# Performance work log

Hardware: AMD Instinct MI355X
Metric: run time of the kernel (lower is better)

The kernel has to match this reference:

```python
import jax, jax.numpy as jnp
import numpy as np

B, S, D, H = 2, 2048, 1024, 16
HW = D // H  # head width = 64
MASK_FILL = -100000000.0


def setup_inputs() -> dict:
    key0 = jax.random.key(0)
    ks = jax.random.split(key0, 12)
    inp = {
        "query": jax.random.normal(ks[0], (B, S, D), jnp.float32),
        "key": jax.random.normal(ks[1], (B, S, D), jnp.float32),
        "value": jax.random.normal(ks[2], (B, S, D), jnp.float32),
        # bool mask, True masks; broadcasts over batch and heads
        "mask": jax.random.randint(ks[3], (S, S), 0, 2).astype(jnp.bool_),
        # per-head projection kernels: (heads, head_width, d_in)
        "Wq": jax.random.normal(ks[4], (H, HW, D), jnp.float32) * 0.02,
        "bq": jnp.zeros((H, HW), jnp.float32),
        "Wk": jax.random.normal(ks[5], (H, HW, D), jnp.float32) * 0.02,
        "bk": jnp.zeros((H, HW), jnp.float32),
        "Wv": jax.random.normal(ks[6], (H, HW, D), jnp.float32) * 0.02,
        "bv": jnp.zeros((H, HW), jnp.float32),
        # collapse projector: contracts (heads, head_width) -> d_output
        "Wo": jax.random.normal(ks[7], (D, H, HW), jnp.float32) * 0.02,
        "bo": jnp.zeros((D,), jnp.float32),
    }
    return inp


def reference(query, key, value, mask, Wq, bq, Wk, bk, Wv, bv, Wo, bo):
    # head projections -> (b, h, s, w)
    q = jnp.einsum("bsd,hwd->bhsw", query, Wq) + bq[:, None, :]
    k = jnp.einsum("btd,hwd->bhtw", key, Wk) + bk[:, None, :]
    v = jnp.einsum("btd,hwd->bhtw", value, Wv) + bv[:, None, :]
    # unscaled logits, masked_fill, softmax (matches original exactly)
    logits = jnp.einsum("bhsw,bhtw->bhst", q, k)
    logits = jnp.where(mask, MASK_FILL, logits)
    score = jax.nn.softmax(logits, axis=-1)
    # NOTE: original divides AV output by sqrt(head_width) AFTER softmax
    attn = jnp.einsum("bhst,bhtw->bhsw", score, v) / jnp.sqrt(jnp.float32(HW))
    # collapse heads -> (b, s, d_output)
    out = jnp.einsum("bhsw,ohw->bso", attn, Wo) + bo
    return out
```

## Files before the change

kernel.cpp:

```cpp
#include <hip/hip_runtime.h>
#include <hip/hip_bf16.h>
#include <math.h>

#define S_LEN   2048
#define D_MODEL 1024
#define N_HEADS 16
#define HEAD_W  64
#define BATCH   2
#define MROWS   (BATCH * S_LEN)
#define MASK_FILL -100000000.0f
#define LOG2E 1.4426950408889634f

typedef __attribute__((ext_vector_type(8))) short bf16x8;
typedef __attribute__((ext_vector_type(4))) float f32x4;
typedef unsigned short u16;
typedef unsigned int   u32;
typedef unsigned long long u64;

__device__ __forceinline__ u16 f2bf(float f) {
    u32 u = __float_as_uint(f);
    return (u16)((u + 0x7fffu + ((u >> 16) & 1u)) >> 16);
}

__device__ __forceinline__ u32 pack_bf16x2(float lo, float hi) {
    __hip_bfloat162 t = __float22bfloat162_rn(make_float2(lo, hi));
    u32 r;
    __builtin_memcpy(&r, &t, 4);
    return r;
}

__device__ __forceinline__ void gld_lds16(const void* gp, void* lp) {
    __builtin_amdgcn_global_load_lds(
        (const __attribute__((address_space(1))) u32*)gp,
        (__attribute__((address_space(3))) u32*)lp, 16, 0, 0);
}

struct CvtJobs {
    const float* src[7];
    u16* dst[7];
    int n[7];
};
__global__ __launch_bounds__(256) void prep_kernel(
    CvtJobs j, const unsigned char* __restrict__ mask, u64* __restrict__ bits) {
    const int t = blockIdx.y;
    if (t < 7) {
        const float* s = j.src[t];
        u16* d = j.dst[t];
        const int n = j.n[t];
        int i = (blockIdx.x * 256 + threadIdx.x) * 4;
        if (i < n) {
            float4 v = *(const float4*)(s + i);
            ushort4 o;
            o.x = f2bf(v.x); o.y = f2bf(v.y); o.z = f2bf(v.z); o.w = f2bf(v.w);
            *(ushort4*)(d + i) = o;
        }
        return;
    }
    if (blockIdx.x >= 2048) return;
    __shared__ int isByte;
    if (threadIdx.x == 0) isByte = 0;
    __syncthreads();
    const int e0 = blockIdx.x * 2048;
    const uint2 v = ((const uint2*)(mask + e0))[threadIdx.x];
    if (((v.x | v.y) & 0xFFFFFF00u) != 0u) isByte = 1;
    __syncthreads();
    const int ib = isByte;
    const int* mi = (const int*)mask;
#pragma unroll
    for (int jj = 0; jj < 8; ++jj) {
        const int e = e0 + jj * 256 + threadIdx.x;
        const bool m = ib ? (mask[e] != 0) : (mi[e] != 0);
        const u64 bl = __ballot(m);
        if ((e & 63) == 0) bits[e >> 6] = bl;
    }
}

__device__ __forceinline__ void gemm_core_bf16(const u16* __restrict__ A,
                                               const u16* __restrict__ Bt,
                                               int m0, int n0, f32x4 acc[4][4]) {
    __shared__ u16 As[2][4096];
    __shared__ u16 Bs[2][4096];
    const int tid = threadIdx.x;
    const int wv = tid >> 6, ln = tid & 63;
    const int lane16 = ln & 15, quad = ln >> 4;
    const int wr = (wv >> 1) * 64, wc = (wv & 1) * 64;
    const u16* A0 = A + (size_t)(m0 + ln) * D_MODEL + wv * 8;
    const u16* A1 = A + (size_t)(m0 + 64 + ln) * D_MODEL + wv * 8;
    const u16* B0 = Bt + (size_t)(n0 + ln) * D_MODEL + wv * 8;
    const u16* B1 = Bt + (size_t)(n0 + 64 + ln) * D_MODEL + wv * 8;

    gld_lds16(A0, &As[0][wv * 1024]);
    gld_lds16(A1, &As[0][wv * 1024 + 512]);
    gld_lds16(B0, &Bs[0][wv * 1024]);
    gld_lds16(B1, &Bs[0][wv * 1024 + 512]);

    for (int kt = 0; kt < D_MODEL / 32; ++kt) {
        const int buf = kt & 1;
        __syncthreads();
        if (kt < D_MODEL / 32 - 1) {
            const int ko = (kt + 1) * 32;
            gld_lds16(A0 + ko, &As[buf ^ 1][wv * 1024]);
            gld_lds16(A1 + ko, &As[buf ^ 1][wv * 1024 + 512]);
            gld_lds16(B0 + ko, &Bs[buf ^ 1][wv * 1024]);
            gld_lds16(B1 + ko, &Bs[buf ^ 1][wv * 1024 + 512]);
        }
        bf16x8 af[4], bfv[4];
#pragma unroll
        for (int mt = 0; mt < 4; ++mt)
            af[mt] = *(const bf16x8*)&As[buf][quad * 1024 + (wr + mt * 16 + lane16) * 8];
#pragma unroll
        for (int nt = 0; nt < 4; ++nt)
            bfv[nt] = *(const bf16x8*)&Bs[buf][quad * 1024 + (wc + nt * 16 + lane16) * 8];
#pragma unroll
        for (int mt = 0; mt < 4; ++mt)
#pragma unroll
            for (int nt = 0; nt < 4; ++nt)
                acc[mt][nt] = __builtin_amdgcn_mfma_f32_16x16x32_bf16(
                    af[mt], bfv[nt], acc[mt][nt], 0, 0, 0);
    }
}

__global__ __launch_bounds__(256, 4) void qkv_gemm_kernel(
    const u16* __restrict__ xq, const u16* __restrict__ xk, const u16* __restrict__ xv,
    const u16* __restrict__ wq, const u16* __restrict__ wk, const u16* __restrict__ wv,
    const float* __restrict__ bq, const float* __restrict__ bk, const float* __restrict__ bv,
    u16* __restrict__ qb, u16* __restrict__ kb, u16* __restrict__ vtmp) {
    const u16* A; const u16* Bt; const float* bias; u16* outp;
    const int z = blockIdx.z;
    if (z == 0)      { A = xq; Bt = wq; bias = bq; outp = qb; }
    else if (z == 1) { A = xk; Bt = wk; bias = bk; outp = kb; }
    else             { A = xv; Bt = wv; bias = bv; outp = vtmp; }
    f32x4 acc[4][4] = {};
    const int m0 = blockIdx.y * 128, n0 = blockIdx.x * 128;
    gemm_core_bf16(A, Bt, m0, n0, acc);

    const int tid = threadIdx.x;
    const int wvi = tid >> 6, ln = tid & 63;
    const int lane16 = ln & 15, quad = ln >> 4;
    const int wr = (wvi >> 1) * 64, wc = (wvi & 1) * 64;
    const float scale = (z == 0) ? LOG2E : 1.0f;
#pragma unroll
    for (int nt = 0; nt < 4; ++nt) {
        const int n = n0 + wc + nt * 16 + lane16;
        const float bb = bias[n];
        const int h = n >> 6, w = n & 63;
#pragma unroll
        for (int mt = 0; mt < 4; ++mt)
#pragma unroll
            for (int r = 0; r < 4; ++r) {
                const int m = m0 + wr + mt * 16 + quad * 4 + r;
                const int bidx = m >> 11, s = m & 2047;
                outp[((size_t)((bidx * N_HEADS + h) * S_LEN + s)) * HEAD_W + w] =
                    f2bf((acc[mt][nt][r] + bb) * scale);
            }
    }
}

__global__ __launch_bounds__(256) void vtrans_kernel(
    const u16* __restrict__ vtmp, u16* __restrict__ vbt) {
    __shared__ u16 T[64][72];
    const int tid = threadIdx.x;
    const int bh = blockIdx.y;
    const int s0 = blockIdx.x * 64;
    const int row = tid >> 2, seg = (tid & 3) * 16;
    const u16* src = vtmp + ((size_t)bh * S_LEN + s0 + row) * HEAD_W + seg;
    uint4 a = *(const uint4*)src;
    uint4 b2 = *(const uint4*)(src + 8);
    u16 tmp[16];
    *(uint4*)tmp = a; *(uint4*)(tmp + 8) = b2;
#pragma unroll
    for (int j = 0; j < 16; ++j) T[seg + j][row] = tmp[j];
    __syncthreads();
    u16* dst = vbt + ((size_t)bh * HEAD_W + row) * S_LEN + s0 + seg;
    *(uint4*)dst       = *(const uint4*)&T[row][seg];
    *(uint4*)(dst + 8) = *(const uint4*)&T[row][seg + 8];
}

__global__ __launch_bounds__(256, 4) void out_gemm_kernel(
    const u16* __restrict__ ab, const u16* __restrict__ wo,
    const float* __restrict__ bo, float* __restrict__ out) {
    f32x4 acc[4][4] = {};
    const int m0 = blockIdx.y * 128, n0 = blockIdx.x * 128;
    gemm_core_bf16(ab, wo, m0, n0, acc);
    const int tid = threadIdx.x;
    const int wvi = tid >> 6, ln = tid & 63;
    const int lane16 = ln & 15, quad = ln >> 4;
    const int wr = (wvi >> 1) * 64, wc = (wvi & 1) * 64;
#pragma unroll
    for (int nt = 0; nt < 4; ++nt) {
        const int n = n0 + wc + nt * 16 + lane16;
        const float bb = bo[n];
#pragma unroll
        for (int mt = 0; mt < 4; ++mt)
#pragma unroll
            for (int r = 0; r < 4; ++r) {
                const int m = m0 + wr + mt * 16 + quad * 4 + r;
                out[(size_t)m * D_MODEL + n] = acc[mt][nt][r] + bb;
            }
    }
}

__global__ __launch_bounds__(256, 3) void attn_kernel(
    const u16* __restrict__ qbuf, const u16* __restrict__ kbuf,
    const u16* __restrict__ vbt, const u64* __restrict__ mbits,
    float* __restrict__ Opart, float* __restrict__ lpart) {
    __shared__ u16 Ks[2][4096];
    __shared__ u16 Vt[2][4096];
    __shared__ u16 Ps[4][32 * 72];
    const int tid = threadIdx.x;
    const int wv = tid >> 6, ln = tid & 63;
    const int lane16 = ln & 15, quad = ln >> 4;
    const int s_blk = blockIdx.x * 128;
    const int h = blockIdx.y;
    const int b = blockIdx.z >> 1, hf = blockIdx.z & 1;
    const int c0 = hf * 16;
    const size_t hb = ((size_t)(b * N_HEADS + h)) * S_LEN * HEAD_W;
    const u16* Qg = qbuf + hb;
    const u16* Kg = kbuf + hb;
    const u16* Vg = vbt + hb;

    bf16x8 qa[2][2];
#pragma unroll
    for (int mt = 0; mt < 2; ++mt)
#pragma unroll
        for (int kk = 0; kk < 2; ++kk)
            qa[mt][kk] = *(const bf16x8*)(Qg +
                (size_t)(s_blk + wv * 32 + mt * 16 + lane16) * HEAD_W + kk * 32 + quad * 8);

    const size_t mrow0 = (size_t)(s_blk + wv * 32 + lane16) * 32;
    const size_t mrow1 = (size_t)(s_blk + wv * 32 + 16 + lane16) * 32;
    u64 mwCur0 = mbits[mrow0 + c0], mwCur1 = mbits[mrow1 + c0];
    u64 mwNx0 = 0, mwNx1 = 0;

    {
        const int t0g = c0 * 64;
        const int i0 = 2 * wv, i1 = 2 * wv + 1;
        gld_lds16(Kg + (size_t)(t0g + ln) * HEAD_W + i0 * 8, &Ks[0][i0 * 512]);
        gld_lds16(Kg + (size_t)(t0g + ln) * HEAD_W + i1 * 8, &Ks[0][i1 * 512]);
        gld_lds16(Vg + (size_t)ln * S_LEN + t0g + i0 * 8, &Vt[0][i0 * 512]);
        gld_lds16(Vg + (size_t)ln * S_LEN + t0g + i1 * 8, &Vt[0][i1 * 512]);
    }

    f32x4 oacc[2][4] = {};
    float lsum[2] = {0.0f, 0.0f};

    for (int ci = 0; ci < 16; ++ci) {
        const int c = c0 + ci;
        const int buf = ci & 1;
        __syncthreads();
        if (ci < 15) {
            const int t1 = (c + 1) * 64;
            const int i0 = 2 * wv, i1 = 2 * wv + 1;
            gld_lds16(Kg + (size_t)(t1 + ln) * HEAD_W + i0 * 8, &Ks[buf ^ 1][i0 * 512]);
            gld_lds16(Kg + (size_t)(t1 + ln) * HEAD_W + i1 * 8, &Ks[buf ^ 1][i1 * 512]);
            gld_lds16(Vg + (size_t)ln * S_LEN + t1 + i0 * 8, &Vt[buf ^ 1][i0 * 512]);
            gld_lds16(Vg + (size_t)ln * S_LEN + t1 + i1 * 8, &Vt[buf ^ 1][i1 * 512]);
            mwNx0 = mbits[mrow0 + c + 1];
            mwNx1 = mbits[mrow1 + c + 1];
        }

        f32x4 st[4][2] = {};
#pragma unroll
        for (int kk = 0; kk < 2; ++kk)
#pragma unroll
            for (int ntT = 0; ntT < 4; ++ntT) {
                bf16x8 kf = *(const bf16x8*)&Ks[buf][(kk * 4 + quad) * 512 + (ntT * 16 + lane16) * 8];
#pragma unroll
                for (int mt = 0; mt < 2; ++mt)
                    st[ntT][mt] = __builtin_amdgcn_mfma_f32_16x16x32_bf16(
                        kf, qa[mt][kk], st[ntT][mt], 0, 0, 0);
            }

#pragma unroll
        for (int mt = 0; mt < 2; ++mt) {
            const u64 mw = mt ? mwCur1 : mwCur0;
            float ls0 = 0.0f, ls1 = 0.0f;
#pragma unroll
            for (int ntT = 0; ntT < 4; ++ntT) {
                const u32 nib = (u32)(mw >> (ntT * 16 + quad * 4)) & 15u;
                float p0 = exp2f(st[ntT][mt][0]); if (nib & 1u) p0 = 0.0f;
                float p1 = exp2f(st[ntT][mt][1]); if (nib & 2u) p1 = 0.0f;
                float p2 = exp2f(st[ntT][mt][2]); if (nib & 4u) p2 = 0.0f;
                float p3 = exp2f(st[ntT][mt][3]); if (nib & 8u) p3 = 0.0f;
                ls0 += p0 + p1;
                ls1 += p2 + p3;
                uint2 pk;
                pk.x = pack_bf16x2(p0, p1);
                pk.y = pack_bf16x2(p2, p3);
                *(uint2*)&Ps[wv][(mt * 16 + lane16) * 72 + ntT * 16 + quad * 4] = pk;
            }
            lsum[mt] += ls0 + ls1;
        }

        bf16x8 pf[2][2];
#pragma unroll
        for (int mt = 0; mt < 2; ++mt)
#pragma unroll
            for (int kk = 0; kk < 2; ++kk)
                pf[mt][kk] = *(const bf16x8*)&Ps[wv][(mt * 16 + lane16) * 72 + kk * 32 + quad * 8];
#pragma unroll
        for (int kk = 0; kk < 2; ++kk)
#pragma unroll
            for (int ntw = 0; ntw < 4; ++ntw) {
                bf16x8 vf = *(const bf16x8*)&Vt[buf][(kk * 4 + quad) * 512 + (ntw * 16 + lane16) * 8];
#pragma unroll
                for (int mt = 0; mt < 2; ++mt)
                    oacc[mt][ntw] = __builtin_amdgcn_mfma_f32_16x16x32_bf16(
                        pf[mt][kk], vf, oacc[mt][ntw], 0, 0, 0);
            }
        mwCur0 = mwNx0; mwCur1 = mwNx1;
    }

    float* OpB = Opart + ((size_t)(hf * 4096 + b * 2048)) * 1024;
#pragma unroll
    for (int mt = 0; mt < 2; ++mt) {
#pragma unroll
        for (int r = 0; r < 4; ++r) {
            const int s = s_blk + wv * 32 + mt * 16 + quad * 4 + r;
            float* dst = OpB + (size_t)s * 1024 + h * 64;
#pragma unroll
            for (int ntw = 0; ntw < 4; ++ntw)
                dst[ntw * 16 + lane16] = oacc[mt][ntw][r];
        }
        float lm = lsum[mt];
        lm += __shfl_xor(lm, 16);
        lm += __shfl_xor(lm, 32);
        if (quad == 0) {
            const int srow = s_blk + wv * 32 + mt * 16 + lane16;
            lpart[(size_t)(hf * 4096 + b * 2048 + srow) * 16 + h] = lm;
        }
    }
}

__global__ __launch_bounds__(256) void combine_kernel(
    const float* __restrict__ Op, const float* __restrict__ lp,
    u16* __restrict__ ab) {
    const int idx4 = blockIdx.x * 256 + threadIdx.x;
    const int row = idx4 >> 8;
    const int d = (idx4 & 255) * 4;
    const int h = d >> 6;
    const float l = lp[(size_t)row * 16 + h] + lp[(size_t)(4096 + row) * 16 + h];
    const float inv = 0.125f / l;
    float4 a = *(const float4*)(Op + (size_t)row * 1024 + d);
    float4 b = *(const float4*)(Op + (size_t)(4096 + row) * 1024 + d);
    ushort4 o;
    o.x = f2bf((a.x + b.x) * inv);
    o.y = f2bf((a.y + b.y) * inv);
    o.z = f2bf((a.z + b.z) * inv);
    o.w = f2bf((a.w + b.w) * inv);
    *(ushort4*)(ab + (size_t)row * 1024 + d) = o;
}

extern "C" void kernel_launch(void* const* d_in, const int* in_sizes, int n_in,
                              void* d_out, int out_size, void* d_ws, size_t ws_size,
                              hipStream_t stream) {
    const float* query = (const float*)d_in[0];
    const float* key   = (const float*)d_in[1];
    const float* value = (const float*)d_in[2];
    const void*  mask  = d_in[3];
    const float* Wq = (const float*)d_in[4];
    const float* bq = (const float*)d_in[5];
    const float* Wk = (const float*)d_in[6];
    const float* bk = (const float*)d_in[7];
    const float* Wv = (const float*)d_in[8];
    const float* bv = (const float*)d_in[9];
    const float* Wo = (const float*)d_in[10];
    const float* bo = (const float*)d_in[11];
    float* out = (float*)d_out;

    char* ws = (char*)d_ws;
    const size_t MB = 1024 * 1024;
    u64* bits = (u64*)ws;
    u16* wob  = (u16*)(ws + 1 * MB);
    u16* qb   = (u16*)(ws + 3 * MB);
    u16* kb   = (u16*)(ws + 11 * MB);
    u16* vbt  = (u16*)(ws + 19 * MB);
    char* uA = ws + 27 * MB;
    u16* xq   = (u16*)(uA);
    u16* xk   = (u16*)(uA + 8 * MB);
    u16* xv   = (u16*)(uA + 16 * MB);
    u16* wqb  = (u16*)(uA + 24 * MB);
    u16* wkb  = (u16*)(uA + 26 * MB);
    u16* wvb  = (u16*)(uA + 28 * MB);
    u16* vtmp = (u16*)(uA + 30 * MB);
    float* Opart = (float*)(uA);
    float* lpart = (float*)(uA + 32 * MB);
    u16* ab = qb;

    const size_t NACT = (size_t)MROWS * D_MODEL;
    const size_t NW   = (size_t)D_MODEL * D_MODEL;

    CvtJobs j;
    j.src[0] = query; j.dst[0] = xq;  j.n[0] = (int)NACT;
    j.src[1] = key;   j.dst[1] = xk;  j.n[1] = (int)NACT;
    j.src[2] = value; j.dst[2] = xv;  j.n[2] = (int)NACT;
    j.src[3] = Wq;    j.dst[3] = wqb; j.n[3] = (int)NW;
    j.src[4] = Wk;    j.dst[4] = wkb; j.n[4] = (int)NW;
    j.src[5] = Wv;    j.dst[5] = wvb; j.n[5] = (int)NW;
    j.src[6] = Wo;    j.dst[6] = wob; j.n[6] = (int)NW;
    prep_kernel<<<dim3(NACT / 1024, 8), 256, 0, stream>>>(
        j, (const unsigned char*)mask, bits);

    qkv_gemm_kernel<<<dim3(D_MODEL / 128, MROWS / 128, 3), 256, 0, stream>>>(
        xq, xk, xv, wqb, wkb, wvb, bq, bk, bv, qb, kb, vtmp);
    vtrans_kernel<<<dim3(S_LEN / 64, BATCH * N_HEADS), 256, 0, stream>>>(vtmp, vbt);
    attn_kernel<<<dim3(S_LEN / 128, N_HEADS, BATCH * 2), 256, 0, stream>>>(
        qb, kb, vbt, bits, Opart, lpart);
    combine_kernel<<<4096, 256, 0, stream>>>(Opart, lpart, ab);
    out_gemm_kernel<<<dim3(D_MODEL / 128, MROWS / 128), 256, 0, stream>>>(
        ab, wob, bo, out);
}
```

Baseline: 313.3 us.

## Compute V projection transposed directly and shrink GEMM tiles to 64x128

The V projection is now computed as Wv·xv^T inside the QKV GEMM, so it writes the transposed V layout directly and the separate vtrans kernel plus its intermediate buffer are removed. All projection and output GEMMs switch from 128x128 to 64x128 block tiles, doubling the grid size to improve occupancy and wave count across CUs. Smaller tiles lower per-block arithmetic intensity and raise redundant global loads of the B operand. The transposed V writes are strided along the sequence dimension at lane16 granularity, which may coalesce less well.

```diff
diff --git a/kernel.cpp b/kernel.cpp
--- a/kernel.cpp
+++ b/kernel.cpp
@@ -75,22 +75,20 @@
     }
 }
 
-__device__ __forceinline__ void gemm_core_bf16(const u16* __restrict__ A,
-                                               const u16* __restrict__ Bt,
-                                               int m0, int n0, f32x4 acc[4][4]) {
-    __shared__ u16 As[2][4096];
+__device__ __forceinline__ void gemm_core_64(const u16* __restrict__ A,
+                                             const u16* __restrict__ Bt,
+                                             int m0, int n0, f32x4 acc[2][4]) {
+    __shared__ u16 As[2][2048];
     __shared__ u16 Bs[2][4096];
     const int tid = threadIdx.x;
     const int wv = tid >> 6, ln = tid & 63;
     const int lane16 = ln & 15, quad = ln >> 4;
-    const int wr = (wv >> 1) * 64, wc = (wv & 1) * 64;
-    const u16* A0 = A + (size_t)(m0 + ln) * D_MODEL + wv * 8;
-    const u16* A1 = A + (size_t)(m0 + 64 + ln) * D_MODEL + wv * 8;
+    const int wr = (wv >> 1) * 32, wc = (wv & 1) * 64;
+    const u16* Ap = A + (size_t)(m0 + ln) * D_MODEL + wv * 8;
     const u16* B0 = Bt + (size_t)(n0 + ln) * D_MODEL + wv * 8;
     const u16* B1 = Bt + (size_t)(n0 + 64 + ln) * D_MODEL + wv * 8;
 
-    gld_lds16(A0, &As[0][wv * 1024]);
-    gld_lds16(A1, &As[0][wv * 1024 + 512]);
+    gld_lds16(Ap, &As[0][wv * 512]);
     gld_lds16(B0, &Bs[0][wv * 1024]);
     gld_lds16(B1, &Bs[0][wv * 1024 + 512]);
 
@@ -99,20 +97,19 @@
         __syncthreads();
         if (kt < D_MODEL / 32 - 1) {
             const int ko = (kt + 1) * 32;
-            gld_lds16(A0 + ko, &As[buf ^ 1][wv * 1024]);
-            gld_lds16(A1 + ko, &As[buf ^ 1][wv * 1024 + 512]);
+            gld_lds16(Ap + ko, &As[buf ^ 1][wv * 512]);
             gld_lds16(B0 + ko, &Bs[buf ^ 1][wv * 1024]);
             gld_lds16(B1 + ko, &Bs[buf ^ 1][wv * 1024 + 512]);
         }
-        bf16x8 af[4], bfv[4];
-#pragma unroll
-        for (int mt = 0; mt < 4; ++mt)
-            af[mt] = *(const bf16x8*)&As[buf][quad * 1024 + (wr + mt * 16 + lane16) * 8];
+        bf16x8 af[2], bfv[4];
+#pragma unroll
+        for (int mt = 0; mt < 2; ++mt)
+            af[mt] = *(const bf16x8*)&As[buf][quad * 512 + (wr + mt * 16 + lane16) * 8];
 #pragma unroll
         for (int nt = 0; nt < 4; ++nt)
             bfv[nt] = *(const bf16x8*)&Bs[buf][quad * 1024 + (wc + nt * 16 + lane16) * 8];
 #pragma unroll
-        for (int mt = 0; mt < 4; ++mt)
+        for (int mt = 0; mt < 2; ++mt)
 #pragma unroll
             for (int nt = 0; nt < 4; ++nt)
                 acc[mt][nt] = __builtin_amdgcn_mfma_f32_16x16x32_bf16(
@@ -124,28 +121,50 @@
     const u16* __restrict__ xq, const u16* __restrict__ xk, const u16* __restrict__ xv,
     const u16* __restrict__ wq, const u16* __restrict__ wk, const u16* __restrict__ wv,
     const float* __restrict__ bq, const float* __restrict__ bk, const float* __restrict__ bv,
-    u16* __restrict__ qb, u16* __restrict__ kb, u16* __restrict__ vtmp) {
-    const u16* A; const u16* Bt; const float* bias; u16* outp;
+    u16* __restrict__ qb, u16* __restrict__ kb, u16* __restrict__ vbt) {
     const int z = blockIdx.z;
-    if (z == 0)      { A = xq; Bt = wq; bias = bq; outp = qb; }
-    else if (z == 1) { A = xk; Bt = wk; bias = bk; outp = kb; }
-    else             { A = xv; Bt = wv; bias = bv; outp = vtmp; }
-    f32x4 acc[4][4] = {};
-    const int m0 = blockIdx.y * 128, n0 = blockIdx.x * 128;
-    gemm_core_bf16(A, Bt, m0, n0, acc);
-
     const int tid = threadIdx.x;
     const int wvi = tid >> 6, ln = tid & 63;
     const int lane16 = ln & 15, quad = ln >> 4;
-    const int wr = (wvi >> 1) * 64, wc = (wvi & 1) * 64;
+    const int wr = (wvi >> 1) * 32, wc = (wvi & 1) * 64;
+    f32x4 acc[2][4] = {};
+
+    if (z == 2) {
+        const int m0 = (blockIdx.y & 15) * 64;
+        const int n0 = (((blockIdx.y >> 4) * 8) + blockIdx.x) * 128;
+        gemm_core_64(wv, xv, m0, n0, acc);
+#pragma unroll
+        for (int mt = 0; mt < 2; ++mt)
+#pragma unroll
+            for (int r = 0; r < 4; ++r) {
+                const int m = m0 + wr + mt * 16 + quad * 4 + r;
+                const int h = m >> 6, w = m & 63;
+                const float bb = bv[m];
+#pragma unroll
+                for (int nt = 0; nt < 4; ++nt) {
+                    const int n = n0 + wc + nt * 16 + lane16;
+                    const int bidx = n >> 11, t = n & 2047;
+                    vbt[((size_t)((bidx * N_HEADS + h) * HEAD_W + w)) * S_LEN + t] =
+                        f2bf(acc[mt][nt][r] + bb);
+                }
+            }
+        return;
+    }
+
+    const u16* A = (z == 0) ? xq : xk;
+    const u16* Bt = (z == 0) ? wq : wk;
+    const float* bias = (z == 0) ? bq : bk;
+    u16* outp = (z == 0) ? qb : kb;
     const float scale = (z == 0) ? LOG2E : 1.0f;
+    const int m0 = blockIdx.y * 64, n0 = blockIdx.x * 128;
+    gemm_core_64(A, Bt, m0, n0, acc);
 #pragma unroll
     for (int nt = 0; nt < 4; ++nt) {
         const int n = n0 + wc + nt * 16 + lane16;
         const float bb = bias[n];
         const int h = n >> 6, w = n & 63;
 #pragma unroll
-        for (int mt = 0; mt < 4; ++mt)
+        for (int mt = 0; mt < 2; ++mt)
 #pragma unroll
             for (int r = 0; r < 4; ++r) {
                 const int m = m0 + wr + mt * 16 + quad * 4 + r;
@@ -156,42 +175,22 @@
     }
 }
 
-__global__ __launch_bounds__(256) void vtrans_kernel(
-    const u16* __restrict__ vtmp, u16* __restrict__ vbt) {
-    __shared__ u16 T[64][72];
-    const int tid = threadIdx.x;
-    const int bh = blockIdx.y;
-    const int s0 = blockIdx.x * 64;
-    const int row = tid >> 2, seg = (tid & 3) * 16;
-    const u16* src = vtmp + ((size_t)bh * S_LEN + s0 + row) * HEAD_W + seg;
-    uint4 a = *(const uint4*)src;
-    uint4 b2 = *(const uint4*)(src + 8);
-    u16 tmp[16];
-    *(uint4*)tmp = a; *(uint4*)(tmp + 8) = b2;
-#pragma unroll
-    for (int j = 0; j < 16; ++j) T[seg + j][row] = tmp[j];
-    __syncthreads();
-    u16* dst = vbt + ((size_t)bh * HEAD_W + row) * S_LEN + s0 + seg;
-    *(uint4*)dst       = *(const uint4*)&T[row][seg];
-    *(uint4*)(dst + 8) = *(const uint4*)&T[row][seg + 8];
-}
-
 __global__ __launch_bounds__(256, 4) void out_gemm_kernel(
     const u16* __restrict__ ab, const u16* __restrict__ wo,
     const float* __restrict__ bo, float* __restrict__ out) {
-    f32x4 acc[4][4] = {};
-    const int m0 = blockIdx.y * 128, n0 = blockIdx.x * 128;
-    gemm_core_bf16(ab, wo, m0, n0, acc);
+    f32x4 acc[2][4] = {};
+    const int m0 = blockIdx.y * 64, n0 = blockIdx.x * 128;
+    gemm_core_64(ab, wo, m0, n0, acc);
     const int tid = threadIdx.x;
     const int wvi = tid >> 6, ln = tid & 63;
     const int lane16 = ln & 15, quad = ln >> 4;
-    const int wr = (wvi >> 1) * 64, wc = (wvi & 1) * 64;
+    const int wr = (wvi >> 1) * 32, wc = (wvi & 1) * 64;
 #pragma unroll
     for (int nt = 0; nt < 4; ++nt) {
         const int n = n0 + wc + nt * 16 + lane16;
         const float bb = bo[n];
 #pragma unroll
-        for (int mt = 0; mt < 4; ++mt)
+        for (int mt = 0; mt < 2; ++mt)
 #pragma unroll
             for (int r = 0; r < 4; ++r) {
                 const int m = m0 + wr + mt * 16 + quad * 4 + r;
@@ -382,7 +381,6 @@
     u16* wqb  = (u16*)(uA + 24 * MB);
     u16* wkb  = (u16*)(uA + 26 * MB);
     u16* wvb  = (u16*)(uA + 28 * MB);
-    u16* vtmp = (u16*)(uA + 30 * MB);
     float* Opart = (float*)(uA);
     float* lpart = (float*)(uA + 32 * MB);
     u16* ab = qb;
@@ -401,12 +399,11 @@
     prep_kernel<<<dim3(NACT / 1024, 8), 256, 0, stream>>>(
         j, (const unsigned char*)mask, bits);
 
-    qkv_gemm_kernel<<<dim3(D_MODEL / 128, MROWS / 128, 3), 256, 0, stream>>>(
-        xq, xk, xv, wqb, wkb, wvb, bq, bk, bv, qb, kb, vtmp);
-    vtrans_kernel<<<dim3(S_LEN / 64, BATCH * N_HEADS), 256, 0, stream>>>(vtmp, vbt);
+    qkv_gemm_kernel<<<dim3(D_MODEL / 128, MROWS / 64, 3), 256, 0, stream>>>(
+        xq, xk, xv, wqb, wkb, wvb, bq, bk, bv, qb, kb, vbt);
     attn_kernel<<<dim3(S_LEN / 128, N_HEADS, BATCH * 2), 256, 0, stream>>>(
         qb, kb, vbt, bits, Opart, lpart);
     combine_kernel<<<4096, 256, 0, stream>>>(Opart, lpart, ab);
-    out_gemm_kernel<<<dim3(D_MODEL / 128, MROWS / 128), 256, 0, stream>>>(
+    out_gemm_kernel<<<dim3(D_MODEL / 128, MROWS / 64), 256, 0, stream>>>(
         ab, wob, bo, out);
 }
```

Measured after the change: 326.2 us. 4.1% more time.
